# Kernel tuning notes

Measured on AMD Instinct MI355X. Metric: run time of the kernel, lower is better.

Reference implementation:

```python
import jax, jax.numpy as jnp
import numpy as np

HIDDEN = 1024
HEADS = 16
BATCH = 2
SEQ = 2048
# dropout_p = 0.1 but module evaluated in eval mode (training=False) -> identity


def setup_inputs() -> dict:
    key = jax.random.key(0)
    k1, k2, k3 = jax.random.split(key, 3)
    x = jax.random.normal(k1, (BATCH, SEQ, HIDDEN), dtype=jnp.float32)
    # unit-scaling Linear: weight ~ N(0,1) (reset_parameters uses nn.init.normal_)
    w_qkv = jax.random.normal(k2, (3 * HIDDEN, HIDDEN), dtype=jnp.float32)
    w_o = jax.random.normal(k3, (HIDDEN, HIDDEN), dtype=jnp.float32)
    return {"x": x, "w_qkv": w_qkv, "w_o": w_o}


def reference(x, w_qkv, w_o):
    b, s, hid = x.shape
    heads = HEADS
    d = hid // heads
    # unit-scaled linear (constraint='to_output_scale'): y = x @ W.T * fan_in**-0.5
    qkv = (x @ w_qkv.T) * (hid ** -0.5)            # [b, s, 3*hid]
    # einops 'b s (z h d) -> z b h s d'
    qkv = qkv.reshape(b, s, 3, heads, d)
    q = jnp.transpose(qkv[:, :, 0], (0, 2, 1, 3))   # [b, h, s, d]
    k = jnp.transpose(qkv[:, :, 1], (0, 2, 1, 3))
    v = jnp.transpose(qkv[:, :, 2], (0, 2, 1, 3))
    # unit-scaled matmul: scale = inner_dim**-0.5
    scores = jnp.einsum('bhqd,bhkd->bhqk', q, k) * (d ** -0.5)  # [b, h, s, s]
    # unit-scaled softmax: output_scale = n / sqrt(n - 1)
    attn = jax.nn.softmax(scores, axis=-1) * (s / np.sqrt(s - 1.0))
    # dropout inactive (eval mode)
    out = jnp.einsum('bhqk,bhkd->bhqd', attn, v) * (s ** -0.5)  # inner dim = s
    out = jnp.transpose(out, (0, 2, 1, 3)).reshape(b, s, hid)   # 'b h s d -> b s (h d)'
    return (out @ w_o.T) * (hid ** -0.5)
```

## Files before the change

kernel.cpp:

```cpp
#include <hip/hip_runtime.h>

typedef unsigned short u16;
typedef _Float16 f16x8 __attribute__((ext_vector_type(8)));
typedef _Float16 f16x4 __attribute__((ext_vector_type(4)));
typedef _Float16 f16x2 __attribute__((ext_vector_type(2)));
typedef float f32x4 __attribute__((ext_vector_type(4)));
typedef unsigned short u16x4 __attribute__((ext_vector_type(4)));

#define HID 1024
#define SEQ 2048
#define NH 16
#define DH 64

__device__ __forceinline__ u16 f2h(float f) {
  return __builtin_bit_cast(u16, (_Float16)f);
}
__device__ __forceinline__ f32x4 mfma_h(f16x8 a, f16x8 b, f32x4 c) {
  return __builtin_amdgcn_mfma_f32_16x16x32_f16(a, b, c, 0, 0, 0);
}
__device__ __forceinline__ f32x4 mfma_h16(f16x4 a, f16x4 b, f32x4 c) {
  return __builtin_amdgcn_mfma_f32_16x16x16f16(a, b, c, 0, 0, 0);
}
__device__ __forceinline__ float fexp2(float x) {
#if __has_builtin(__builtin_amdgcn_exp2f)
  return __builtin_amdgcn_exp2f(x);
#else
  return __expf(0.69314718f * x);
#endif
}
__device__ __forceinline__ f16x2 pkrtz(float a, float b) {
  return __builtin_bit_cast(f16x2, __builtin_amdgcn_cvt_pkrtz(a, b));
}
__device__ __forceinline__ void g2l16(const u16* g, u16* l) {
  __builtin_amdgcn_global_load_lds(
      (const __attribute__((address_space(1))) unsigned int*)g,
      (__attribute__((address_space(3))) unsigned int*)l, 16, 0, 0);
}

#define NX4 ((4096 * 1024) / 4)
#define NQ4 ((3072 * 1024) / 4)
#define NO4 ((1024 * 1024) / 4)
__global__ __launch_bounds__(256) void prep_kernel(
    const float* __restrict__ x, const float* __restrict__ wq,
    const float* __restrict__ wo,
    u16* __restrict__ x16, u16* __restrict__ wq16, u16* __restrict__ wo16) {
  int i = blockIdx.x * 256 + threadIdx.x;
  const float4 v = (i < NX4) ? ((const float4*)x)[i]
                 : (i < NX4 + NQ4) ? ((const float4*)wq)[i - NX4]
                 : ((const float4*)wo)[i - NX4 - NQ4];
  u16* dst = (i < NX4) ? &x16[(size_t)i * 4]
           : (i < NX4 + NQ4) ? &wq16[(size_t)(i - NX4) * 4]
           : &wo16[(size_t)(i - NX4 - NQ4) * 4];
  u16x4 o;
  o[0] = f2h(v.x); o[1] = f2h(v.y); o[2] = f2h(v.z); o[3] = f2h(v.w);
  *(u16x4*)dst = o;
}

__global__ __launch_bounds__(256, 3) void gemm_qkv(
    const u16* __restrict__ a16, const u16* __restrict__ b16,
    u16* __restrict__ qf, u16* __restrict__ kf, u16* __restrict__ vtf) {
  __shared__ __align__(16) u16 la[128 * 64], lb[128 * 64];
  const int t = threadIdx.x;
  const int lane = t & 63, w = t >> 6;
  const int wr = w >> 1, wc = w & 1;
  const int lr = lane & 15, lg = lane >> 4;
  const int br = blockIdx.x, bc = blockIdx.y;
  const f32x4 fzero = {0.f, 0.f, 0.f, 0.f};
  f32x4 acc[4][4];
#pragma unroll
  for (int i = 0; i < 4; ++i)
#pragma unroll
    for (int j = 0; j < 4; ++j) acc[i][j] = fzero;
  const int srow = t >> 3, scol = ((t & 7) ^ (srow & 7)) << 3;
  const u16* ga = a16 + (size_t)(br * 128 + srow) * HID + scol;
  const u16* gb = b16 + (size_t)(bc * 128 + srow) * HID + scol;
  const int lo16 = t * 8;
  for (int kk = 0; kk < HID; kk += 64) {
#pragma unroll
    for (int r = 0; r < 4; ++r)
      g2l16(ga + kk + (size_t)(r * 32) * HID, &la[lo16 + r * 2048]);
#pragma unroll
    for (int r = 0; r < 4; ++r)
      g2l16(gb + kk + (size_t)(r * 32) * HID, &lb[lo16 + r * 2048]);
    __syncthreads();
#pragma unroll
    for (int ks = 0; ks < 2; ++ks) {
      f16x8 ah[4], bh[4];
#pragma unroll
      for (int i = 0; i < 4; ++i) {
        int row = wr * 64 + i * 16 + lr;
        ah[i] = *(const f16x8*)&la[row * 64 + (((ks * 4 + lg) ^ (row & 7)) << 3)];
      }
#pragma unroll
      for (int j = 0; j < 4; ++j) {
        int row = wc * 64 + j * 16 + lr;
        bh[j] = *(const f16x8*)&lb[row * 64 + (((ks * 4 + lg) ^ (row & 7)) << 3)];
      }
#pragma unroll
      for (int i = 0; i < 4; ++i)
#pragma unroll
        for (int j = 0; j < 4; ++j) acc[i][j] = mfma_h(ah[i], bh[j], acc[i][j]);
    }
    __syncthreads();
  }
  const int m0 = br * 128 + wr * 64, n0 = bc * 128 + wc * 64;
#pragma unroll
  for (int i = 0; i < 4; ++i)
#pragma unroll
    for (int j = 0; j < 4; ++j)
#pragma unroll
      for (int r = 0; r < 4; ++r) {
        int row = m0 + i * 16 + lg * 4 + r;
        int col = n0 + j * 16 + lr;
        float val = acc[i][j][r] * 0.03125f;
        int b = row >> 11, s = row & 2047;
        int z = col >> 10, hh = (col >> 6) & 15, d = col & 63;
        int bhid = b * NH + hh;
        if (z == 0) {
          qf[((size_t)bhid * SEQ + s) * DH + d] = f2h(val * 0.18033688f);
        } else if (z == 1) {
          kf[((size_t)bhid * SEQ + s) * DH + d] = f2h(val);
        } else {
          int kv = s & 63;
          int ct = kv >> 4, lgv = (kv >> 2) & 3, rv = kv & 3;
          int kvp = ((ct >> 1) << 5) | (lgv << 3) | ((ct & 1) << 2) | rv;
          int s2 = (s & ~63) | kvp;
          vtf[((size_t)bhid * DH + d) * SEQ + s2] = f2h(val);
        }
      }
}

__global__ __launch_bounds__(256, 2) void gemm_proj(
    const u16* __restrict__ a16, const u16* __restrict__ b16,
    float* __restrict__ out) {
  __shared__ __align__(16) u16 la[128 * 64];
  __shared__ __align__(16) u16 lb[64 * 64];
  const int t = threadIdx.x;
  const int lane = t & 63, w = t >> 6;
  const int wr = w >> 1, wc = w & 1;
  const int lr = lane & 15, lg = lane >> 4;
  const int br = blockIdx.x, bc = blockIdx.y;
  const f32x4 fzero = {0.f, 0.f, 0.f, 0.f};
  f32x4 acc[4][2];
#pragma unroll
  for (int i = 0; i < 4; ++i)
#pragma unroll
    for (int j = 0; j < 2; ++j) acc[i][j] = fzero;
  const int srow = t >> 3, scol = ((t & 7) ^ (srow & 7)) << 3;
  const u16* ga = a16 + (size_t)(br * 128 + srow) * HID + scol;
  const u16* gb = b16 + (size_t)(bc * 64 + srow) * HID + scol;
  const int lo16 = t * 8;
  for (int kk = 0; kk < HID; kk += 64) {
#pragma unroll
    for (int r = 0; r < 4; ++r)
      g2l16(ga + kk + (size_t)(r * 32) * HID, &la[lo16 + r * 2048]);
#pragma unroll
    for (int r = 0; r < 2; ++r)
      g2l16(gb + kk + (size_t)(r * 32) * HID, &lb[lo16 + r * 2048]);
    __syncthreads();
#pragma unroll
    for (int ks = 0; ks < 2; ++ks) {
      f16x8 ah[4], bh[2];
#pragma unroll
      for (int i = 0; i < 4; ++i) {
        int row = wr * 64 + i * 16 + lr;
        ah[i] = *(const f16x8*)&la[row * 64 + (((ks * 4 + lg) ^ (row & 7)) << 3)];
      }
#pragma unroll
      for (int j = 0; j < 2; ++j) {
        int row = wc * 32 + j * 16 + lr;
        bh[j] = *(const f16x8*)&lb[row * 64 + (((ks * 4 + lg) ^ (row & 7)) << 3)];
      }
#pragma unroll
      for (int i = 0; i < 4; ++i)
#pragma unroll
        for (int j = 0; j < 2; ++j)
          acc[i][j] = mfma_h(ah[i], bh[j], acc[i][j]);
    }
    __syncthreads();
  }
  const int m0 = br * 128 + wr * 64, n0 = bc * 64 + wc * 32;
#pragma unroll
  for (int i = 0; i < 4; ++i)
#pragma unroll
    for (int j = 0; j < 2; ++j)
#pragma unroll
      for (int r = 0; r < 4; ++r) {
        int row = m0 + i * 16 + lg * 4 + r;
        int col = n0 + j * 16 + lr;
        out[(size_t)row * HID + col] = acc[i][j][r] * 0.03125f;
      }
}

__global__ __launch_bounds__(256, 2) void attn_kernel(
    const u16* __restrict__ qf, const u16* __restrict__ kf,
    const u16* __restrict__ vtf, u16* __restrict__ o16) {
  __shared__ __align__(16) u16 lk[2][64 * 64];
  __shared__ __align__(16) u16 lv[2][64 * 64];
  const int t = threadIdx.x;
  const int lane = t & 63, w = t >> 6;
  const int lr = lane & 15, lg = lane >> 4;
  const int bh = blockIdx.x, qt = blockIdx.y;
  const size_t base_qk = (size_t)bh * SEQ * DH;
  const size_t base_vt = (size_t)bh * DH * SEQ;

  f16x8 qfr[2][2];
#pragma unroll
  for (int rt = 0; rt < 2; ++rt)
#pragma unroll
    for (int ks = 0; ks < 2; ++ks)
      qfr[rt][ks] = *(const f16x8*)&qf[base_qk +
          (size_t)(qt * 128 + w * 32 + rt * 16 + lr) * DH + ks * 32 + lg * 8];

  f16x4 bI;
#pragma unroll
  for (int j = 0; j < 4; ++j) bI[j] = (_Float16)((lr == lg * 4 + j) ? 1.0f : 0.0f);

  const f32x4 fzero = {0.f, 0.f, 0.f, 0.f};
  f32x4 acc_o[2][4];
  float l_i[2][4];
#pragma unroll
  for (int rt = 0; rt < 2; ++rt)
#pragma unroll
    for (int r = 0; r < 4; ++r) l_i[rt][r] = 0.f;
#pragma unroll
  for (int rt = 0; rt < 2; ++rt)
#pragma unroll
    for (int ct = 0; ct < 4; ++ct) acc_o[rt][ct] = fzero;

  const int srow = t >> 3;
  const int scol = ((t & 7) ^ (srow & 7)) << 3;
  const int lo16 = t * 8;

  const u16* gk0 = kf + base_qk + (size_t)srow * DH + scol;
  const u16* gv0 = vtf + base_vt + (size_t)srow * SEQ + scol;

#define STAGE(buf, j)                                             \
  {                                                               \
    const u16* gk = gk0 + (size_t)(j) * 64 * DH;                  \
    g2l16(gk, &lk[buf][lo16]);                                    \
    g2l16(gk + 32 * DH, &lk[buf][lo16 + 2048]);                   \
    const u16* gv = gv0 + (j) * 64;                               \
    g2l16(gv, &lv[buf][lo16]);                                    \
    g2l16(gv + (size_t)32 * SEQ, &lv[buf][lo16 + 2048]);          \
  }

  STAGE(0, 0)

  for (int j = 0; j < SEQ / 64; ++j) {
    const int cur = j & 1;
    __syncthreads();

    f32x4 sa[2][4];
#pragma unroll
    for (int rt = 0; rt < 2; ++rt)
#pragma unroll
      for (int ct = 0; ct < 4; ++ct) sa[rt][ct] = fzero;
    __builtin_amdgcn_s_setprio(1);
#pragma unroll
    for (int ks = 0; ks < 2; ++ks)
#pragma unroll
      for (int ct = 0; ct < 4; ++ct) {
        int row = ct * 16 + lr;
        f16x8 kfr = *(const f16x8*)&lk[cur][row * 64 + (((ks * 4 + lg) ^ (row & 7)) << 3)];
#pragma unroll
        for (int rt = 0; rt < 2; ++rt) sa[rt][ct] = mfma_h(qfr[rt][ks], kfr, sa[rt][ct]);
      }
    __builtin_amdgcn_s_setprio(0);

    if (j + 1 < SEQ / 64) STAGE(cur ^ 1, j + 1)

    f16x8 pfr[2][2];
#pragma unroll
    for (int rt = 0; rt < 2; ++rt) {
      f32x4 tr[4];
#pragma unroll
      for (int ct = 0; ct < 4; ++ct) {
        float p0 = fexp2(sa[rt][ct][0]);
        float p1 = fexp2(sa[rt][ct][1]);
        float p2 = fexp2(sa[rt][ct][2]);
        float p3 = fexp2(sa[rt][ct][3]);
        l_i[rt][0] += p0; l_i[rt][1] += p1;
        l_i[rt][2] += p2; l_i[rt][3] += p3;
        union { f16x2 h2[2]; f16x4 h4; } ua;
        ua.h2[0] = pkrtz(p0, p1);
        ua.h2[1] = pkrtz(p2, p3);
        tr[ct] = mfma_h16(ua.h4, bI, fzero);
      }
#pragma unroll
      for (int ks = 0; ks < 2; ++ks) {
        union { f16x2 h2[4]; f16x8 h8; } up;
        up.h2[0] = pkrtz(tr[ks * 2][0], tr[ks * 2][1]);
        up.h2[1] = pkrtz(tr[ks * 2][2], tr[ks * 2][3]);
        up.h2[2] = pkrtz(tr[ks * 2 + 1][0], tr[ks * 2 + 1][1]);
        up.h2[3] = pkrtz(tr[ks * 2 + 1][2], tr[ks * 2 + 1][3]);
        pfr[rt][ks] = up.h8;
      }
    }

    __builtin_amdgcn_s_setprio(1);
#pragma unroll
    for (int ks = 0; ks < 2; ++ks)
#pragma unroll
      for (int ct = 0; ct < 4; ++ct) {
        int vrow = ct * 16 + lr;
        f16x8 vfr = *(const f16x8*)&lv[cur][vrow * 64 + (((ks * 4 + lg) ^ (vrow & 7)) << 3)];
#pragma unroll
        for (int rt = 0; rt < 2; ++rt) acc_o[rt][ct] = mfma_h(pfr[rt][ks], vfr, acc_o[rt][ct]);
      }
    __builtin_amdgcn_s_setprio(0);
  }

#pragma unroll
  for (int rt = 0; rt < 2; ++rt)
#pragma unroll
    for (int r = 0; r < 4; ++r) {
      float l = l_i[rt][r];
      l += __shfl_xor(l, 1, 16);
      l += __shfl_xor(l, 2, 16);
      l += __shfl_xor(l, 4, 16);
      l += __shfl_xor(l, 8, 16);
      l_i[rt][r] = l;
    }

  const int b = bh >> 4, hh = bh & 15;
  const float fact = 1.00024426f;
#pragma unroll
  for (int rt = 0; rt < 2; ++rt)
#pragma unroll
    for (int r = 0; r < 4; ++r) {
      float inv = fact / l_i[rt][r];
      int s = qt * 128 + w * 32 + rt * 16 + lg * 4 + r;
#pragma unroll
      for (int ct = 0; ct < 4; ++ct) {
        int d = ct * 16 + lr;
        float val = acc_o[rt][ct][r] * inv;
        o16[((size_t)(b * SEQ + s)) * HID + hh * DH + d] = f2h(val);
      }
    }
}

extern "C" void kernel_launch(void* const* d_in, const int* in_sizes, int n_in,
                              void* d_out, int out_size, void* d_ws, size_t ws_size,
                              hipStream_t stream) {
  const float* x = (const float*)d_in[0];
  const float* w_qkv = (const float*)d_in[1];
  const float* w_o = (const float*)d_in[2];
  u16* ws = (u16*)d_ws;
  const size_t XS = (size_t)4096 * 1024;
  const size_t WQ = (size_t)3072 * 1024;
  const size_t WO = (size_t)1024 * 1024;
  u16* x16  = ws;           u16* wq16 = x16 + XS;
  u16* wo16 = wq16 + WQ;
  u16* q_f  = wo16 + WO;    u16* k_f  = q_f + XS;
  u16* vt_f = k_f + XS;     u16* o16  = vt_f + XS;

  prep_kernel<<<(NX4 + NQ4 + NO4) / 256, 256, 0, stream>>>(
      x, w_qkv, w_o, x16, wq16, wo16);
  gemm_qkv<<<dim3(32, 24), 256, 0, stream>>>(x16, wq16, q_f, k_f, vt_f);
  attn_kernel<<<dim3(32, 16), 256, 0, stream>>>(q_f, k_f, vt_f, o16);
  gemm_proj<<<dim3(32, 16), 256, 0, stream>>>(o16, wo16, (float*)d_out);
}
```

Baseline: 169.3 us.

## Software-pipeline QK and PV across tiles, compute row sums via MFMA

Restructures the attention loop so the QK^T score tile for the next K block is computed while the softmax and PV product of the previous block run, with K and V staged separately into double buffers. The row-sum of probabilities is moved from scalar adds plus a cross-lane shuffle reduction onto extra MFMAs against a ones vector. The aim is to overlap matrix and exponent work and cut VALU work, at the cost of more registers (two score tiles live) and extra MFMA issues. Because the sum now uses the fp16-rounded probabilities, it matches the values fed into the PV product.

```diff
diff --git a/kernel.cpp b/kernel.cpp
--- a/kernel.cpp
+++ b/kernel.cpp
@@ -215,18 +215,19 @@
   f16x4 bI;
 #pragma unroll
   for (int j = 0; j < 4; ++j) bI[j] = (_Float16)((lr == lg * 4 + j) ? 1.0f : 0.0f);
+  f16x8 vones;
+#pragma unroll
+  for (int j = 0; j < 8; ++j) vones[j] = (_Float16)1.0f;
 
   const f32x4 fzero = {0.f, 0.f, 0.f, 0.f};
   f32x4 acc_o[2][4];
-  float l_i[2][4];
-#pragma unroll
-  for (int rt = 0; rt < 2; ++rt)
-#pragma unroll
-    for (int r = 0; r < 4; ++r) l_i[rt][r] = 0.f;
-#pragma unroll
-  for (int rt = 0; rt < 2; ++rt)
+  f32x4 acc_l[2];
+#pragma unroll
+  for (int rt = 0; rt < 2; ++rt) {
+    acc_l[rt] = fzero;
 #pragma unroll
     for (int ct = 0; ct < 4; ++ct) acc_o[rt][ct] = fzero;
+  }
 
   const int srow = t >> 3;
   const int scol = ((t & 7) ^ (srow & 7)) << 3;
@@ -235,41 +236,35 @@
   const u16* gk0 = kf + base_qk + (size_t)srow * DH + scol;
   const u16* gv0 = vtf + base_vt + (size_t)srow * SEQ + scol;
 
-#define STAGE(buf, j)                                             \
-  {                                                               \
-    const u16* gk = gk0 + (size_t)(j) * 64 * DH;                  \
-    g2l16(gk, &lk[buf][lo16]);                                    \
-    g2l16(gk + 32 * DH, &lk[buf][lo16 + 2048]);                   \
-    const u16* gv = gv0 + (j) * 64;                               \
-    g2l16(gv, &lv[buf][lo16]);                                    \
-    g2l16(gv + (size_t)32 * SEQ, &lv[buf][lo16 + 2048]);          \
-  }
-
-  STAGE(0, 0)
-
-  for (int j = 0; j < SEQ / 64; ++j) {
-    const int cur = j & 1;
-    __syncthreads();
-
-    f32x4 sa[2][4];
-#pragma unroll
-    for (int rt = 0; rt < 2; ++rt)
-#pragma unroll
-      for (int ct = 0; ct < 4; ++ct) sa[rt][ct] = fzero;
+  auto STAGE_K = [&](int buf, int j) {
+    const u16* gk = gk0 + (size_t)j * 64 * DH;
+    g2l16(gk, &lk[buf][lo16]);
+    g2l16(gk + 32 * DH, &lk[buf][lo16 + 2048]);
+  };
+  auto STAGE_V = [&](int buf, int j) {
+    const u16* gv = gv0 + j * 64;
+    g2l16(gv, &lv[buf][lo16]);
+    g2l16(gv + (size_t)32 * SEQ, &lv[buf][lo16 + 2048]);
+  };
+
+  f32x4 saA[2][4], saB[2][4];
+
+  auto QK_TILE = [&](f32x4 (&sa)[2][4], const u16* lkb) {
     __builtin_amdgcn_s_setprio(1);
 #pragma unroll
-    for (int ks = 0; ks < 2; ++ks)
-#pragma unroll
-      for (int ct = 0; ct < 4; ++ct) {
-        int row = ct * 16 + lr;
-        f16x8 kfr = *(const f16x8*)&lk[cur][row * 64 + (((ks * 4 + lg) ^ (row & 7)) << 3)];
-#pragma unroll
-        for (int rt = 0; rt < 2; ++rt) sa[rt][ct] = mfma_h(qfr[rt][ks], kfr, sa[rt][ct]);
-      }
+    for (int ct = 0; ct < 4; ++ct) {
+      int row = ct * 16 + lr;
+      f16x8 k0 = *(const f16x8*)&lkb[row * 64 + ((lg ^ (row & 7)) << 3)];
+      f16x8 k1 = *(const f16x8*)&lkb[row * 64 + (((4 + lg) ^ (row & 7)) << 3)];
+      sa[0][ct] = mfma_h(qfr[0][0], k0, fzero);
+      sa[1][ct] = mfma_h(qfr[1][0], k0, fzero);
+      sa[0][ct] = mfma_h(qfr[0][1], k1, sa[0][ct]);
+      sa[1][ct] = mfma_h(qfr[1][1], k1, sa[1][ct]);
+    }
     __builtin_amdgcn_s_setprio(0);
-
-    if (j + 1 < SEQ / 64) STAGE(cur ^ 1, j + 1)
-
+  };
+
+  auto SM_PV = [&](f32x4 (&sa)[2][4], const u16* lvb) {
     f16x8 pfr[2][2];
 #pragma unroll
     for (int rt = 0; rt < 2; ++rt) {
@@ -280,8 +275,6 @@
         float p1 = fexp2(sa[rt][ct][1]);
         float p2 = fexp2(sa[rt][ct][2]);
         float p3 = fexp2(sa[rt][ct][3]);
-        l_i[rt][0] += p0; l_i[rt][1] += p1;
-        l_i[rt][2] += p2; l_i[rt][3] += p3;
         union { f16x2 h2[2]; f16x4 h4; } ua;
         ua.h2[0] = pkrtz(p0, p1);
         ua.h2[1] = pkrtz(p2, p3);
@@ -297,31 +290,49 @@
         pfr[rt][ks] = up.h8;
       }
     }
-
     __builtin_amdgcn_s_setprio(1);
 #pragma unroll
     for (int ks = 0; ks < 2; ++ks)
 #pragma unroll
       for (int ct = 0; ct < 4; ++ct) {
         int vrow = ct * 16 + lr;
-        f16x8 vfr = *(const f16x8*)&lv[cur][vrow * 64 + (((ks * 4 + lg) ^ (vrow & 7)) << 3)];
+        f16x8 vfr = *(const f16x8*)&lvb[vrow * 64 + (((ks * 4 + lg) ^ (vrow & 7)) << 3)];
 #pragma unroll
         for (int rt = 0; rt < 2; ++rt) acc_o[rt][ct] = mfma_h(pfr[rt][ks], vfr, acc_o[rt][ct]);
       }
+#pragma unroll
+    for (int rt = 0; rt < 2; ++rt) {
+      acc_l[rt] = mfma_h(pfr[rt][0], vones, acc_l[rt]);
+      acc_l[rt] = mfma_h(pfr[rt][1], vones, acc_l[rt]);
+    }
     __builtin_amdgcn_s_setprio(0);
+  };
+
+  STAGE_K(0, 0);
+  STAGE_V(0, 0);
+  STAGE_K(1, 1);
+  __syncthreads();
+  QK_TILE(saA, lk[0]);
+
+  for (int n = 0; n < 30; n += 2) {
+    __syncthreads();
+    STAGE_V(1, n + 1);
+    STAGE_K(0, n + 2);
+    QK_TILE(saB, lk[1]);
+    SM_PV(saA, lv[0]);
+
+    __syncthreads();
+    STAGE_V(0, n + 2);
+    STAGE_K(1, n + 3);
+    QK_TILE(saA, lk[0]);
+    SM_PV(saB, lv[1]);
   }
-
-#pragma unroll
-  for (int rt = 0; rt < 2; ++rt)
-#pragma unroll
-    for (int r = 0; r < 4; ++r) {
-      float l = l_i[rt][r];
-      l += __shfl_xor(l, 1, 16);
-      l += __shfl_xor(l, 2, 16);
-      l += __shfl_xor(l, 4, 16);
-      l += __shfl_xor(l, 8, 16);
-      l_i[rt][r] = l;
-    }
+  __syncthreads();
+  STAGE_V(1, 31);
+  QK_TILE(saB, lk[1]);
+  SM_PV(saA, lv[0]);
+  __syncthreads();
+  SM_PV(saB, lv[1]);
 
   const int b = bh >> 4, hh = bh & 15;
   const float fact = 1.00024426f;
@@ -329,7 +340,7 @@
   for (int rt = 0; rt < 2; ++rt)
 #pragma unroll
     for (int r = 0; r < 4; ++r) {
-      float inv = fact / l_i[rt][r];
+      float inv = fact / acc_l[rt][r];
       int s = qt * 128 + w * 32 + rt * 16 + lg * 4 + r;
 #pragma unroll
       for (int ct = 0; ct < 4; ++ct) {
```

Result: slower. 177.1 us (+4.6%).
